# Kernel optimization log

Hardware: AMD Instinct MI355X
Metric: run time of the kernel (lower is better)

The kernel has to match this reference:

```python
import jax, jax.numpy as jnp
import numpy as np

B, S, D, H = 4, 512, 128, 8


def setup_inputs() -> dict:
    key = jax.random.key(0)
    k = jax.random.split(key, 5)
    # torch Linear(2D->D): weight [D, 2D]; we store transposed [2D, D] for x @ W
    w1 = jax.random.normal(k[0], (2 * D, D), jnp.float32) / np.sqrt(2 * D)
    b1 = jnp.zeros((D,), jnp.float32)
    w2 = jax.random.normal(k[1], (D, H), jnp.float32) / np.sqrt(D)
    b2 = jnp.zeros((H,), jnp.float32)
    node_features = jax.random.normal(k[2], (B, S, D), jnp.float32)
    return {"node_features": node_features, "w1": w1, "b1": b1, "w2": w2, "b2": b2}


def reference(node_features, w1, b1, w2, b2):
    # concat([x_i, x_j]) @ w1 == x_i @ w1[:D] + x_j @ w1[D:]  (exact same math,
    # avoids materializing the [B,S,S,2D] concatenated tensor)
    a = jnp.einsum('bsd,de->bse', node_features, w1[:D])   # row (i) projection
    c = jnp.einsum('bsd,de->bse', node_features, w1[D:])   # col (j) projection
    h = jax.nn.relu(a[:, :, None, :] + c[:, None, :, :] + b1)  # [B,S,S,D]
    e = jax.nn.sigmoid(jnp.einsum('bijd,dh->bijh', h, w2) + b2)  # [B,S,S,H]
    return jnp.transpose(e, (0, 3, 1, 2))  # [B,H,S,S]
```

## Files before the change

kernel.cpp:

```cpp
#include <hip/hip_runtime.h>
#include <hip/hip_bf16.h>

#define D_ 128
#define S_ 512
#define B_ 4
#define H_ 8

typedef short bf16x8 __attribute__((ext_vector_type(8)));
typedef unsigned int u32x4 __attribute__((ext_vector_type(4)));
typedef float f32x4 __attribute__((ext_vector_type(4)));
typedef float f32x2 __attribute__((ext_vector_type(2)));

__device__ __forceinline__ short f2bf(float f) {
  __hip_bfloat16 h = __float2bfloat16(f);
  return __builtin_bit_cast(short, h);
}
__device__ __forceinline__ float fsigmoid(float x) {
  return __builtin_amdgcn_rcpf(1.0f + __expf(-x));
}
__device__ __forceinline__ unsigned int cvt_pk_bf16(float lo, float hi) {
  unsigned int r;
  asm("v_cvt_pk_bf16_f32 %0, %1, %2" : "=v"(r) : "v"(lo), "v"(hi));
  return r;
}

__global__ __launch_bounds__(256)
void proj_kernel(const float* __restrict__ x, const float* __restrict__ w1,
                 const float* __restrict__ b1, float* __restrict__ Aq,
                 float* __restrict__ Cq) {
  __shared__ float xs[4 * D_];
  __shared__ f32x4 red[256][5];
  const int t = threadIdx.x;
  const int row0 = blockIdx.x * 4;
  ((float2*)xs)[t] = ((const float2*)(x + row0 * D_))[t];
  __syncthreads();
  const int combo = t & 63;
  const int e4 = (combo & 31) * 4;
  const int half = combo >> 5;
  const int kq = t >> 6;
  const float* w1p = w1 + (half * D_ + kq * 32) * D_ + e4;
  const float* xq = xs + kq * 32;
  f32x4 acc[4] = {};
  #pragma unroll 8
  for (int k = 0; k < 32; ++k) {
    float4 wv = *(const float4*)(w1p + k * D_);
    #pragma unroll
    for (int r = 0; r < 4; ++r) {
      float xv = xq[r * D_ + k];
      acc[r][0] += xv * wv.x; acc[r][1] += xv * wv.y;
      acc[r][2] += xv * wv.z; acc[r][3] += xv * wv.w;
    }
  }
  #pragma unroll
  for (int r = 0; r < 4; ++r) red[t][r] = acc[r];
  __syncthreads();
  const int r = t >> 6;
  const int c2 = t & 63;
  f32x4 s = red[c2][r];
  #pragma unroll
  for (int q = 1; q < 4; ++q) {
    f32x4 v = red[c2 + 64 * q][r];
    s[0] += v[0]; s[1] += v[1]; s[2] += v[2]; s[3] += v[3];
  }
  const int fe4 = (c2 & 31) * 4;
  const int row = row0 + r;
  if ((c2 >> 5) == 0) {
    float4 bv = *(const float4*)(b1 + fe4);
    s[0] += bv.x; s[1] += bv.y; s[2] += bv.z; s[3] += bv.w;
    *(f32x4*)(Aq + row * D_ + fe4) = s;
  } else {
    *(f32x4*)(Cq + row * D_ + fe4) = s;
  }
}

__global__ __launch_bounds__(512, 4)
void edge_kernel(const float* __restrict__ Aq, const float* __restrict__ Cq,
                 const float* __restrict__ w2, const float* __restrict__ b2,
                 float* __restrict__ out) {
  __shared__ short cbf[256 * D_];
  const int t = threadIdx.x;
  const int lane = t & 63;
  const int wid = t >> 6;
  const int b  = blockIdx.x >> 7;
  const int jh = (blockIdx.x >> 6) & 1;
  const int ig = blockIdx.x & 63;
  const int i = ig * 8 + wid;

  {
    const float* cb = Cq + (b * S_ + jh * 256) * D_;
    #pragma unroll
    for (int it = 0; it < 8; ++it) {
      int p = t + it * 512;
      int row = p >> 4;
      int u = p & 15;
      const float* src = cb + row * D_ + u * 8;
      float4 v0 = *(const float4*)(src);
      float4 v1 = *(const float4*)(src + 4);
      u32x4 w;
      w[0] = cvt_pk_bf16(v0.x, v0.y);
      w[1] = cvt_pk_bf16(v0.z, v0.w);
      w[2] = cvt_pk_bf16(v1.x, v1.y);
      w[3] = cvt_pk_bf16(v1.z, v1.w);
      *(u32x4*)(cbf + row * D_ + (u ^ (row & 7)) * 8) = w;
    }
  }

  const int jcol = lane & 15;
  const int lgrp = lane >> 4;
  const int sw = jcol & 7;

  f32x2 apk[4][4];
  {
    const float* Ai = Aq + (b * S_ + i) * D_ + lgrp * 8;
    #pragma unroll
    for (int ch = 0; ch < 4; ++ch) {
      float4 v0 = *(const float4*)(Ai + ch * 32);
      float4 v1 = *(const float4*)(Ai + ch * 32 + 4);
      apk[ch][0][0] = v0.x; apk[ch][0][1] = v0.y;
      apk[ch][1][0] = v0.z; apk[ch][1][1] = v0.w;
      apk[ch][2][0] = v1.x; apk[ch][2][1] = v1.y;
      apk[ch][3][0] = v1.z; apk[ch][3][1] = v1.w;
    }
  }
  bf16x8 w2f[4];
  #pragma unroll
  for (int ch = 0; ch < 4; ++ch) {
    #pragma unroll
    for (int e = 0; e < 8; ++e) {
      float wv = (jcol < H_) ? w2[(ch * 32 + lgrp * 8 + e) * H_ + jcol] : 0.0f;
      w2f[ch][e] = f2bf(wv);
    }
  }
  const float b2v = (jcol < H_) ? b2[jcol] : 0.0f;
  float* outp = out + (((size_t)(b * H_ + (jcol & 7)) * S_ + i) * S_)
                + jh * 256 + lgrp * 4;

  __syncthreads();

  u32x4 cva[4], cvb[4];
  auto LOADT = [&](u32x4 (&dst)[4], int jt) {
    const short* bp = cbf + (jt * 16 + jcol) * D_;
    #pragma unroll
    for (int ch = 0; ch < 4; ++ch)
      dst[ch] = *(const u32x4*)(bp + (((ch * 4 + lgrp) ^ sw) * 8));
  };
  auto COMPUTE = [&](u32x4 (&cv)[4], int jt) {
    f32x4 acc = {0.f, 0.f, 0.f, 0.f};
    #pragma unroll
    for (int ch = 0; ch < 4; ++ch) {
      u32x4 hfd;
      #pragma unroll
      for (int p = 0; p < 4; ++p) {
        unsigned int d = cv[ch][p];
        f32x2 v;
        v[0] = __builtin_bit_cast(float, d << 16);
        v[1] = __builtin_bit_cast(float, d & 0xffff0000u);
        v += apk[ch][p];
        hfd[p] = cvt_pk_bf16(fmaxf(v[0], 0.f), fmaxf(v[1], 0.f));
      }
      bf16x8 hf = __builtin_bit_cast(bf16x8, hfd);
      acc = __builtin_amdgcn_mfma_f32_16x16x32_bf16(hf, w2f[ch], acc, 0, 0, 0);
    }
    if (jcol < H_) {
      float4 o;
      o.x = fsigmoid(acc[0] + b2v);
      o.y = fsigmoid(acc[1] + b2v);
      o.z = fsigmoid(acc[2] + b2v);
      o.w = fsigmoid(acc[3] + b2v);
      *(float4*)(outp + jt * 16) = o;
    }
  };

  LOADT(cva, 0);
  #pragma unroll 1
  for (int jt = 0; jt < 16; jt += 2) {
    LOADT(cvb, jt + 1);
    COMPUTE(cva, jt);
    LOADT(cva, (jt + 2) & 15);
    COMPUTE(cvb, jt + 1);
  }
}

extern "C" void kernel_launch(void* const* d_in, const int* in_sizes, int n_in,
                              void* d_out, int out_size, void* d_ws, size_t ws_size,
                              hipStream_t stream) {
  const float* x  = (const float*)d_in[0];
  const float* w1 = (const float*)d_in[1];
  const float* b1 = (const float*)d_in[2];
  const float* w2 = (const float*)d_in[3];
  const float* b2 = (const float*)d_in[4];
  float* out = (float*)d_out;
  float* Aq = (float*)d_ws;
  float* Cq = Aq + B_ * S_ * D_;
  proj_kernel<<<(B_ * S_) / 4, 256, 0, stream>>>(x, w1, b1, Aq, Cq);
  edge_kernel<<<B_ * 2 * 64, 512, 0, stream>>>(Aq, Cq, w2, b2, out);
}
```

Before: 37.82 us.

## Fuse projection into edge kernel, computing column projection with MFMA in LDS

Removes the separate projection kernel and its global Aq/Cq workspace round-trip. Each block now loads raw x for its 256 columns into LDS as bf16, projects them through the second half of w1 with MFMA, and writes the result back into the same LDS tile. The row projection for the block's 8 rows is computed with scalar FMAs. The cost is that every block recomputes the column projection, 64 times redundantly per batch half, and bf16 rounding is now applied to x and w1 as well.

```diff
diff --git a/kernel.cpp b/kernel.cpp
--- a/kernel.cpp
+++ b/kernel.cpp
@@ -24,77 +24,34 @@
   return r;
 }
 
-__global__ __launch_bounds__(256)
-void proj_kernel(const float* __restrict__ x, const float* __restrict__ w1,
-                 const float* __restrict__ b1, float* __restrict__ Aq,
-                 float* __restrict__ Cq) {
-  __shared__ float xs[4 * D_];
-  __shared__ f32x4 red[256][5];
-  const int t = threadIdx.x;
-  const int row0 = blockIdx.x * 4;
-  ((float2*)xs)[t] = ((const float2*)(x + row0 * D_))[t];
-  __syncthreads();
-  const int combo = t & 63;
-  const int e4 = (combo & 31) * 4;
-  const int half = combo >> 5;
-  const int kq = t >> 6;
-  const float* w1p = w1 + (half * D_ + kq * 32) * D_ + e4;
-  const float* xq = xs + kq * 32;
-  f32x4 acc[4] = {};
-  #pragma unroll 8
-  for (int k = 0; k < 32; ++k) {
-    float4 wv = *(const float4*)(w1p + k * D_);
-    #pragma unroll
-    for (int r = 0; r < 4; ++r) {
-      float xv = xq[r * D_ + k];
-      acc[r][0] += xv * wv.x; acc[r][1] += xv * wv.y;
-      acc[r][2] += xv * wv.z; acc[r][3] += xv * wv.w;
-    }
-  }
-  #pragma unroll
-  for (int r = 0; r < 4; ++r) red[t][r] = acc[r];
-  __syncthreads();
-  const int r = t >> 6;
-  const int c2 = t & 63;
-  f32x4 s = red[c2][r];
-  #pragma unroll
-  for (int q = 1; q < 4; ++q) {
-    f32x4 v = red[c2 + 64 * q][r];
-    s[0] += v[0]; s[1] += v[1]; s[2] += v[2]; s[3] += v[3];
-  }
-  const int fe4 = (c2 & 31) * 4;
-  const int row = row0 + r;
-  if ((c2 >> 5) == 0) {
-    float4 bv = *(const float4*)(b1 + fe4);
-    s[0] += bv.x; s[1] += bv.y; s[2] += bv.z; s[3] += bv.w;
-    *(f32x4*)(Aq + row * D_ + fe4) = s;
-  } else {
-    *(f32x4*)(Cq + row * D_ + fe4) = s;
-  }
-}
-
 __global__ __launch_bounds__(512, 4)
-void edge_kernel(const float* __restrict__ Aq, const float* __restrict__ Cq,
-                 const float* __restrict__ w2, const float* __restrict__ b2,
-                 float* __restrict__ out) {
+void fused_kernel(const float* __restrict__ x, const float* __restrict__ w1,
+                  const float* __restrict__ b1, const float* __restrict__ w2,
+                  const float* __restrict__ b2, float* __restrict__ out) {
   __shared__ short cbf[256 * D_];
+  __shared__ float xi[8 * D_];
+  __shared__ float alds[8 * D_];
+
   const int t = threadIdx.x;
   const int lane = t & 63;
   const int wid = t >> 6;
   const int b  = blockIdx.x >> 7;
   const int jh = (blockIdx.x >> 6) & 1;
   const int ig = blockIdx.x & 63;
-  const int i = ig * 8 + wid;
+  const int i  = ig * 8 + wid;
+
+  const int jcol = lane & 15;
+  const int lgrp = lane >> 4;
+  const int sw = jcol & 7;
 
   {
-    const float* cb = Cq + (b * S_ + jh * 256) * D_;
+    const float* xb = x + (b * S_ + jh * 256) * D_;
     #pragma unroll
     for (int it = 0; it < 8; ++it) {
       int p = t + it * 512;
-      int row = p >> 4;
-      int u = p & 15;
-      const float* src = cb + row * D_ + u * 8;
-      float4 v0 = *(const float4*)(src);
+      int row = p >> 4, u = p & 15;
+      const float* src = xb + row * D_ + u * 8;
+      float4 v0 = *(const float4*)src;
       float4 v1 = *(const float4*)(src + 4);
       u32x4 w;
       w[0] = cvt_pk_bf16(v0.x, v0.y);
@@ -103,23 +60,82 @@
       w[3] = cvt_pk_bf16(v1.z, v1.w);
       *(u32x4*)(cbf + row * D_ + (u ^ (row & 7)) * 8) = w;
     }
-  }
-
-  const int jcol = lane & 15;
-  const int lgrp = lane >> 4;
-  const int sw = jcol & 7;
+    const float* xr = x + (size_t)(b * S_ + ig * 8 + wid) * D_;
+    *(float2*)(xi + wid * D_ + lane * 2) = *(const float2*)(xr + lane * 2);
+  }
+  __syncthreads();
+
+  {
+    const int ec = wid * 16 + (lane & 15);
+    const int r1 = lane >> 4;
+    float a0 = 0.f, a1 = 0.f;
+    #pragma unroll 8
+    for (int k = 0; k < D_; ++k) {
+      float wv = w1[k * D_ + ec];
+      a0 += xi[r1 * D_ + k] * wv;
+      a1 += xi[(r1 + 4) * D_ + k] * wv;
+    }
+    float bb = b1[ec];
+    alds[r1 * D_ + ec] = a0 + bb;
+    alds[(r1 + 4) * D_ + ec] = a1 + bb;
+  }
+
+  const int eg = wid * 16 + jcol;
+
+  bf16x8 w1cf[4];
+  #pragma unroll
+  for (int kc = 0; kc < 4; ++kc) {
+    #pragma unroll
+    for (int e = 0; e < 8; ++e)
+      w1cf[kc][e] = f2bf(w1[(D_ + kc * 32 + lgrp * 8 + e) * D_ + eg]);
+  }
+
+  f32x4 dc[8];
+  auto CHALF = [&](int jt0) {
+    #pragma unroll
+    for (int jt = 0; jt < 8; ++jt) {
+      f32x4 acc = {0.f, 0.f, 0.f, 0.f};
+      const short* bp = cbf + ((jt0 + jt) * 16 + jcol) * D_;
+      #pragma unroll
+      for (int kc = 0; kc < 4; ++kc) {
+        u32x4 af = *(const u32x4*)(bp + (((kc * 4 + lgrp) ^ sw) * 8));
+        acc = __builtin_amdgcn_mfma_f32_16x16x32_bf16(
+            __builtin_bit_cast(bf16x8, af), w1cf[kc], acc, 0, 0, 0);
+      }
+      dc[jt] = acc;
+    }
+  };
+  auto CWRITE = [&](int jt0) {
+    const int u = eg >> 3, el = eg & 7;
+    #pragma unroll
+    for (int jt = 0; jt < 8; ++jt) {
+      #pragma unroll
+      for (int reg = 0; reg < 4; ++reg) {
+        int row = (jt0 + jt) * 16 + lgrp * 4 + reg;
+        cbf[row * D_ + ((u ^ (row & 7)) * 8) + el] = f2bf(dc[jt][reg]);
+      }
+    }
+  };
+
+  CHALF(0);
+  __syncthreads();
+  CWRITE(0);
+  __syncthreads();
+  CHALF(8);
+  __syncthreads();
+  CWRITE(8);
 
   f32x2 apk[4][4];
   {
-    const float* Ai = Aq + (b * S_ + i) * D_ + lgrp * 8;
+    const float* Ai = alds + wid * D_ + lgrp * 8;
     #pragma unroll
     for (int ch = 0; ch < 4; ++ch) {
-      float4 v0 = *(const float4*)(Ai + ch * 32);
-      float4 v1 = *(const float4*)(Ai + ch * 32 + 4);
-      apk[ch][0][0] = v0.x; apk[ch][0][1] = v0.y;
-      apk[ch][1][0] = v0.z; apk[ch][1][1] = v0.w;
-      apk[ch][2][0] = v1.x; apk[ch][2][1] = v1.y;
-      apk[ch][3][0] = v1.z; apk[ch][3][1] = v1.w;
+      f32x4 v0 = *(const f32x4*)(Ai + ch * 32);
+      f32x4 v1 = *(const f32x4*)(Ai + ch * 32 + 4);
+      apk[ch][0][0] = v0[0]; apk[ch][0][1] = v0[1];
+      apk[ch][1][0] = v0[2]; apk[ch][1][1] = v0[3];
+      apk[ch][2][0] = v1[0]; apk[ch][2][1] = v1[1];
+      apk[ch][3][0] = v1[2]; apk[ch][3][1] = v1[3];
     }
   }
   bf16x8 w2f[4];
@@ -134,7 +150,6 @@
   const float b2v = (jcol < H_) ? b2[jcol] : 0.0f;
   float* outp = out + (((size_t)(b * H_ + (jcol & 7)) * S_ + i) * S_)
                 + jh * 256 + lgrp * 4;
-
   __syncthreads();
 
   u32x4 cva[4], cvb[4];
@@ -190,8 +205,5 @@
   const float* w2 = (const float*)d_in[3];
   const float* b2 = (const float*)d_in[4];
   float* out = (float*)d_out;
-  float* Aq = (float*)d_ws;
-  float* Cq = Aq + B_ * S_ * D_;
-  proj_kernel<<<(B_ * S_) / 4, 256, 0, stream>>>(x, w1, b1, Aq, Cq);
-  edge_kernel<<<B_ * 2 * 64, 512, 0, stream>>>(Aq, Cq, w2, b2, out);
-}
+  fused_kernel<<<B_ * 2 * 64, 512, 0, stream>>>(x, w1, b1, w2, b2, out);
+}
```

Measured after the change: 40.64 us. 7.5% more time.

## Emit bf16 column projection from proj kernel and read it directly from global

Applied to the files above, without the earlier changes.

The projection kernel now writes the column projection as packed bf16 instead of fp32. The edge kernel drops its 64KB shared-memory staging of the converted tile and the block barrier, and loads each 16-byte chunk straight from global (L2-cached) memory. This removes the per-block fp32 load, conversion and LDS write, and frees LDS, which may allow more resident blocks. In exchange, the inner loop depends on global/L2 load latency instead of LDS latency.

```diff
diff --git a/kernel.cpp b/kernel.cpp
--- a/kernel.cpp
+++ b/kernel.cpp
@@ -27,7 +27,7 @@
 __global__ __launch_bounds__(256)
 void proj_kernel(const float* __restrict__ x, const float* __restrict__ w1,
                  const float* __restrict__ b1, float* __restrict__ Aq,
-                 float* __restrict__ Cq) {
+                 short* __restrict__ Cbf) {
   __shared__ float xs[4 * D_];
   __shared__ f32x4 red[256][5];
   const int t = threadIdx.x;
@@ -69,45 +69,27 @@
     s[0] += bv.x; s[1] += bv.y; s[2] += bv.z; s[3] += bv.w;
     *(f32x4*)(Aq + row * D_ + fe4) = s;
   } else {
-    *(f32x4*)(Cq + row * D_ + fe4) = s;
+    uint2 u;
+    u.x = cvt_pk_bf16(s[0], s[1]);
+    u.y = cvt_pk_bf16(s[2], s[3]);
+    *(uint2*)(Cbf + row * D_ + fe4) = u;
   }
 }
 
 __global__ __launch_bounds__(512, 4)
-void edge_kernel(const float* __restrict__ Aq, const float* __restrict__ Cq,
+void edge_kernel(const float* __restrict__ Aq, const short* __restrict__ Cbf,
                  const float* __restrict__ w2, const float* __restrict__ b2,
                  float* __restrict__ out) {
-  __shared__ short cbf[256 * D_];
   const int t = threadIdx.x;
   const int lane = t & 63;
   const int wid = t >> 6;
   const int b  = blockIdx.x >> 7;
   const int jh = (blockIdx.x >> 6) & 1;
   const int ig = blockIdx.x & 63;
-  const int i = ig * 8 + wid;
-
-  {
-    const float* cb = Cq + (b * S_ + jh * 256) * D_;
-    #pragma unroll
-    for (int it = 0; it < 8; ++it) {
-      int p = t + it * 512;
-      int row = p >> 4;
-      int u = p & 15;
-      const float* src = cb + row * D_ + u * 8;
-      float4 v0 = *(const float4*)(src);
-      float4 v1 = *(const float4*)(src + 4);
-      u32x4 w;
-      w[0] = cvt_pk_bf16(v0.x, v0.y);
-      w[1] = cvt_pk_bf16(v0.z, v0.w);
-      w[2] = cvt_pk_bf16(v1.x, v1.y);
-      w[3] = cvt_pk_bf16(v1.z, v1.w);
-      *(u32x4*)(cbf + row * D_ + (u ^ (row & 7)) * 8) = w;
-    }
-  }
+  const int i  = ig * 8 + wid;
 
   const int jcol = lane & 15;
   const int lgrp = lane >> 4;
-  const int sw = jcol & 7;
 
   f32x2 apk[4][4];
   {
@@ -135,14 +117,14 @@
   float* outp = out + (((size_t)(b * H_ + (jcol & 7)) * S_ + i) * S_)
                 + jh * 256 + lgrp * 4;
 
-  __syncthreads();
+  const short* Cb = Cbf + (b * S_ + jh * 256) * D_ + lgrp * 8;
 
   u32x4 cva[4], cvb[4];
   auto LOADT = [&](u32x4 (&dst)[4], int jt) {
-    const short* bp = cbf + (jt * 16 + jcol) * D_;
+    const short* bp = Cb + (jt * 16 + jcol) * D_;
     #pragma unroll
     for (int ch = 0; ch < 4; ++ch)
-      dst[ch] = *(const u32x4*)(bp + (((ch * 4 + lgrp) ^ sw) * 8));
+      dst[ch] = *(const u32x4*)(bp + ch * 32);
   };
   auto COMPUTE = [&](u32x4 (&cv)[4], int jt) {
     f32x4 acc = {0.f, 0.f, 0.f, 0.f};
@@ -190,8 +172,8 @@
   const float* w2 = (const float*)d_in[3];
   const float* b2 = (const float*)d_in[4];
   float* out = (float*)d_out;
-  float* Aq = (float*)d_ws;
-  float* Cq = Aq + B_ * S_ * D_;
-  proj_kernel<<<(B_ * S_) / 4, 256, 0, stream>>>(x, w1, b1, Aq, Cq);
-  edge_kernel<<<B_ * 2 * 64, 512, 0, stream>>>(Aq, Cq, w2, b2, out);
+  float* Aq  = (float*)d_ws;
+  short* Cbf = (short*)(Aq + B_ * S_ * D_);
+  proj_kernel<<<(B_ * S_) / 4, 256, 0, stream>>>(x, w1, b1, Aq, Cbf);
+  edge_kernel<<<B_ * 2 * 64, 512, 0, stream>>>(Aq, Cbf, w2, b2, out);
 }
```

New measurement: 49.49 us. 30.9% more time.

## Stage C tile in LDS as fp32 with quarter-width j tiles and more blocks

Applied to the files above, without the earlier changes.

The edge kernel now keeps the column projection tile in shared memory as fp32 (swizzled float4 layout) instead of converting it to bf16. To fit, each block covers 128 j columns instead of 256, and the grid doubles to 1024 blocks. The explicit double-buffered LDS register prefetch is replaced by a simple loop that loads directly from shared memory. This removes the bf16 unpack ALU work and raises the block count for better occupancy and balance. In exchange, C is reloaded from global memory twice as often, LDS reads double in bytes, and the software prefetch overlap is lost.

```diff
diff --git a/kernel.cpp b/kernel.cpp
--- a/kernel.cpp
+++ b/kernel.cpp
@@ -77,37 +77,29 @@
 void edge_kernel(const float* __restrict__ Aq, const float* __restrict__ Cq,
                  const float* __restrict__ w2, const float* __restrict__ b2,
                  float* __restrict__ out) {
-  __shared__ short cbf[256 * D_];
+  __shared__ float cs[128 * D_];
   const int t = threadIdx.x;
   const int lane = t & 63;
   const int wid = t >> 6;
-  const int b  = blockIdx.x >> 7;
-  const int jh = (blockIdx.x >> 6) & 1;
+  const int b  = blockIdx.x >> 8;
+  const int jq = (blockIdx.x >> 6) & 3;
   const int ig = blockIdx.x & 63;
-  const int i = ig * 8 + wid;
-
-  {
-    const float* cb = Cq + (b * S_ + jh * 256) * D_;
-    #pragma unroll
-    for (int it = 0; it < 8; ++it) {
-      int p = t + it * 512;
-      int row = p >> 4;
-      int u = p & 15;
-      const float* src = cb + row * D_ + u * 8;
-      float4 v0 = *(const float4*)(src);
-      float4 v1 = *(const float4*)(src + 4);
-      u32x4 w;
-      w[0] = cvt_pk_bf16(v0.x, v0.y);
-      w[1] = cvt_pk_bf16(v0.z, v0.w);
-      w[2] = cvt_pk_bf16(v1.x, v1.y);
-      w[3] = cvt_pk_bf16(v1.z, v1.w);
-      *(u32x4*)(cbf + row * D_ + (u ^ (row & 7)) * 8) = w;
-    }
-  }
+  const int i  = ig * 8 + wid;
 
   const int jcol = lane & 15;
   const int lgrp = lane >> 4;
   const int sw = jcol & 7;
+
+  {
+    const float* cb = Cq + (size_t)(b * S_ + jq * 128) * D_;
+    #pragma unroll
+    for (int it = 0; it < 8; ++it) {
+      int p = t + it * 512;
+      int row = p >> 5, u = p & 31;
+      float4 v = *(const float4*)(cb + row * D_ + u * 4);
+      *(float4*)(cs + row * D_ + ((u ^ (row & 7)) * 4)) = v;
+    }
+  }
 
   f32x2 apk[4][4];
   {
@@ -133,31 +125,29 @@
   }
   const float b2v = (jcol < H_) ? b2[jcol] : 0.0f;
   float* outp = out + (((size_t)(b * H_ + (jcol & 7)) * S_ + i) * S_)
-                + jh * 256 + lgrp * 4;
+                + jq * 128 + lgrp * 4;
 
   __syncthreads();
 
-  u32x4 cva[4], cvb[4];
-  auto LOADT = [&](u32x4 (&dst)[4], int jt) {
-    const short* bp = cbf + (jt * 16 + jcol) * D_;
-    #pragma unroll
-    for (int ch = 0; ch < 4; ++ch)
-      dst[ch] = *(const u32x4*)(bp + (((ch * 4 + lgrp) ^ sw) * 8));
-  };
-  auto COMPUTE = [&](u32x4 (&cv)[4], int jt) {
+  #pragma unroll 1
+  for (int jt = 0; jt < 8; ++jt) {
+    const float* bp = cs + (jt * 16 + jcol) * D_;
     f32x4 acc = {0.f, 0.f, 0.f, 0.f};
     #pragma unroll
     for (int ch = 0; ch < 4; ++ch) {
+      const int u0 = ch * 8 + lgrp * 2;
+      float4 c0 = *(const float4*)(bp + ((u0 ^ sw) * 4));
+      float4 c1 = *(const float4*)(bp + (((u0 + 1) ^ sw) * 4));
       u32x4 hfd;
-      #pragma unroll
-      for (int p = 0; p < 4; ++p) {
-        unsigned int d = cv[ch][p];
-        f32x2 v;
-        v[0] = __builtin_bit_cast(float, d << 16);
-        v[1] = __builtin_bit_cast(float, d & 0xffff0000u);
-        v += apk[ch][p];
-        hfd[p] = cvt_pk_bf16(fmaxf(v[0], 0.f), fmaxf(v[1], 0.f));
-      }
+      f32x2 v;
+      v[0] = c0.x; v[1] = c0.y; v += apk[ch][0];
+      hfd[0] = cvt_pk_bf16(fmaxf(v[0], 0.f), fmaxf(v[1], 0.f));
+      v[0] = c0.z; v[1] = c0.w; v += apk[ch][1];
+      hfd[1] = cvt_pk_bf16(fmaxf(v[0], 0.f), fmaxf(v[1], 0.f));
+      v[0] = c1.x; v[1] = c1.y; v += apk[ch][2];
+      hfd[2] = cvt_pk_bf16(fmaxf(v[0], 0.f), fmaxf(v[1], 0.f));
+      v[0] = c1.z; v[1] = c1.w; v += apk[ch][3];
+      hfd[3] = cvt_pk_bf16(fmaxf(v[0], 0.f), fmaxf(v[1], 0.f));
       bf16x8 hf = __builtin_bit_cast(bf16x8, hfd);
       acc = __builtin_amdgcn_mfma_f32_16x16x32_bf16(hf, w2f[ch], acc, 0, 0, 0);
     }
@@ -169,15 +159,6 @@
       o.w = fsigmoid(acc[3] + b2v);
       *(float4*)(outp + jt * 16) = o;
     }
-  };
-
-  LOADT(cva, 0);
-  #pragma unroll 1
-  for (int jt = 0; jt < 16; jt += 2) {
-    LOADT(cvb, jt + 1);
-    COMPUTE(cva, jt);
-    LOADT(cva, (jt + 2) & 15);
-    COMPUTE(cvb, jt + 1);
   }
 }
 
@@ -193,5 +174,5 @@
   float* Aq = (float*)d_ws;
   float* Cq = Aq + B_ * S_ * D_;
   proj_kernel<<<(B_ * S_) / 4, 256, 0, stream>>>(x, w1, b1, Aq, Cq);
-  edge_kernel<<<B_ * 2 * 64, 512, 0, stream>>>(Aq, Cq, w2, b2, out);
+  edge_kernel<<<B_ * 4 * 64, 512, 0, stream>>>(Aq, Cq, w2, b2, out);
 }
```

After: 37.04 us (median of 2 runs). 2.1% less time.
